# Kernel optimization log

Hardware: AMD Instinct MI355X
Metric: run time of the kernel (lower is better)

The kernel has to match this reference:

```python
import jax, jax.numpy as jnp
import numpy as np

N = 100000
E = 1600000
D_IN = 64
D_OUT = 64

def setup_inputs() -> dict:
    key = jax.random.key(0)
    k1, k2, k3 = jax.random.split(key, 3)
    x = jax.random.normal(k1, (N, D_IN), dtype=jnp.float32)
    edge_index = jax.random.randint(k2, (2, E), 0, N, dtype=jnp.int32)
    W = jax.random.normal(k3, (D_IN, D_OUT), dtype=jnp.float32) * (1.0 / np.sqrt(D_IN))
    b = jnp.zeros((D_OUT,), dtype=jnp.float32)
    return {"x": x, "edge_index": edge_index, "W": W, "b": b}

def reference(x, edge_index, W, b):
    # GCN.forward in eval mode: dropout is identity; GCNConv with
    # normalize=True, add_self_loops=True, edge_weight=None (all ones).
    loop = jnp.arange(N, dtype=edge_index.dtype)
    row = jnp.concatenate([edge_index[0], loop])   # source nodes, [E+N]
    col = jnp.concatenate([edge_index[1], loop])   # target nodes, [E+N]
    ew = jnp.ones(row.shape[0], dtype=x.dtype)
    # symmetric normalization: deg over targets, norm = d^-1/2[row] * d^-1/2[col]
    deg = jax.ops.segment_sum(ew, col, num_segments=N)
    dinv = jnp.where(deg > 0, jax.lax.rsqrt(deg), 0.0)
    norm = dinv[row] * dinv[col]                   # [E+N]
    h = x @ W                                      # [N, D_OUT] dense GEMM first (PyG order)
    msg = h[row] * norm[:, None]                   # gather + scale, [E+N, D_OUT]
    out = jax.ops.segment_sum(msg, col, num_segments=N)  # scatter-add aggregate
    return out + b
```

## Files before the change

kernel.cpp:

```cpp
#include <hip/hip_runtime.h>
#include <hip/hip_fp16.h>
#include <math.h>

constexpr int D = 64;
constexpr int BNODES = 128;
constexpr int BSHIFT = 7;
constexpr int BSTRIDE = 3072;
constexpr int PCHUNK = 4096;
constexpr int NB_MAX = 1024;

typedef _Float16 half8 __attribute__((ext_vector_type(8)));
typedef float floatx4 __attribute__((ext_vector_type(4)));

__global__ __launch_bounds__(256) void k_init(const float* __restrict__ W,
                                              __half* __restrict__ Wt,
                                              int* __restrict__ bcur, int NB) {
    const int i = blockIdx.x * 256 + threadIdx.x;
    if (i < NB) bcur[i] = i * BSTRIDE;
    if (i < D * D) {
        const int j = i >> 6;
        const int k = i & 63;
        Wt[i] = __float2half(W[k * D + j]);
    }
}

__global__ __launch_bounds__(512) void k_partition(
        const int* __restrict__ ei, int* __restrict__ bcur,
        unsigned* __restrict__ ebuf, int E, int NB) {
    __shared__ int lh[NB_MAX];
    __shared__ int lb[NB_MAX];
    __shared__ int cc[PCHUNK];
    const int t = threadIdx.x;
    for (int j = t; j < NB; j += 512) lh[j] = 0;
    __syncthreads();
    const int e0 = blockIdx.x * PCHUNK;
    const int e1 = min(e0 + PCHUNK, E);
    const bool full = (e1 - e0 == PCHUNK);

    if (full) {
        const int4* cp = reinterpret_cast<const int4*>(ei + E + e0);
        const int4 ca = cp[t];
        const int4 cb = cp[t + 512];
        reinterpret_cast<int4*>(cc)[t]       = ca;
        reinterpret_cast<int4*>(cc)[t + 512] = cb;
        atomicAdd(&lh[ca.x >> BSHIFT], 1); atomicAdd(&lh[ca.y >> BSHIFT], 1);
        atomicAdd(&lh[ca.z >> BSHIFT], 1); atomicAdd(&lh[ca.w >> BSHIFT], 1);
        atomicAdd(&lh[cb.x >> BSHIFT], 1); atomicAdd(&lh[cb.y >> BSHIFT], 1);
        atomicAdd(&lh[cb.z >> BSHIFT], 1); atomicAdd(&lh[cb.w >> BSHIFT], 1);
    } else {
        for (int e = e0 + t; e < e1; e += 512) {
            const int c = ei[E + e];
            cc[e - e0] = c;
            atomicAdd(&lh[c >> BSHIFT], 1);
        }
    }
    __syncthreads();
    for (int j = t; j < NB; j += 512) {
        const int n = lh[j];
        lb[j] = n ? atomicAdd(&bcur[j], n) : 0;
        lh[j] = 0;
    }
    __syncthreads();

    if (full) {
        const int4* rp = reinterpret_cast<const int4*>(ei + e0);
        const int4 ra = rp[t];
        const int4 rb = rp[t + 512];
        const int r8[8] = {ra.x, ra.y, ra.z, ra.w, rb.x, rb.y, rb.z, rb.w};
#pragma unroll
        for (int k = 0; k < 8; ++k) {
            const int ci = (k < 4) ? (4 * t + k) : (2048 + 4 * t + (k - 4));
            const int c = cc[ci];
            const int bkt = c >> BSHIFT;
            const int rank = atomicAdd(&lh[bkt], 1);
            const int pos = lb[bkt] + rank;
            if (pos < (bkt + 1) * BSTRIDE)
                ebuf[pos] = ((unsigned)r8[k] << BSHIFT) | (unsigned)(c & (BNODES - 1));
        }
    } else {
        for (int e = e0 + t; e < e1; e += 512) {
            const int r = ei[e];
            const int c = cc[e - e0];
            const int bkt = c >> BSHIFT;
            const int rank = atomicAdd(&lh[bkt], 1);
            const int pos = lb[bkt] + rank;
            if (pos < (bkt + 1) * BSTRIDE)
                ebuf[pos] = ((unsigned)r << BSHIFT) | (unsigned)(c & (BNODES - 1));
        }
    }
}

__global__ __launch_bounds__(512) void k_gemm_fused(
        const float* __restrict__ x, const __half* __restrict__ Wt,
        const unsigned* __restrict__ ebuf, const int* __restrict__ bcur,
        __half* __restrict__ gh, int N) {
    __shared__ int lh[BNODES];
    const int j = blockIdx.x;
    const int t = threadIdx.x;
    const int base = j << BSHIFT;
    const int s0 = j * BSTRIDE;
    const int s1 = min(bcur[j], s0 + BSTRIDE);

    if (t < BNODES) lh[t] = 0;
    __syncthreads();
    for (int i = s0 + t; i < s1; i += 512)
        atomicAdd(&lh[ebuf[i] & (BNODES - 1)], 1);
    __syncthreads();

    const int wave = t >> 6;
    const int node16 = base + wave * 16;
    if (node16 >= N) return;
    const int lane = t & 63;
    const int r16  = lane & 15;
    const int kq   = lane >> 4;

    const _Float16* wt = (const _Float16*)Wt;
    half8 bf[4][2];
#pragma unroll
    for (int jt = 0; jt < 4; ++jt)
#pragma unroll
        for (int s = 0; s < 2; ++s)
            bf[jt][s] = *(const half8*)(wt + (jt * 16 + r16) * D + s * 32 + kq * 8);

    half8 af[2];
#pragma unroll
    for (int s = 0; s < 2; ++s) {
        const float4* xp = reinterpret_cast<const float4*>(
            x + (size_t)(node16 + r16) * D + s * 32 + kq * 8);
        const float4 x0 = xp[0];
        const float4 x1 = xp[1];
        half8 a;
        a[0] = (_Float16)x0.x; a[1] = (_Float16)x0.y;
        a[2] = (_Float16)x0.z; a[3] = (_Float16)x0.w;
        a[4] = (_Float16)x1.x; a[5] = (_Float16)x1.y;
        a[6] = (_Float16)x1.z; a[7] = (_Float16)x1.w;
        af[s] = a;
    }

    floatx4 acc[4];
#pragma unroll
    for (int jt = 0; jt < 4; ++jt) {
        acc[jt] = (floatx4){0.f, 0.f, 0.f, 0.f};
        acc[jt] = __builtin_amdgcn_mfma_f32_16x16x32_f16(af[0], bf[jt][0], acc[jt], 0, 0, 0);
        acc[jt] = __builtin_amdgcn_mfma_f32_16x16x32_f16(af[1], bf[jt][1], acc[jt], 0, 0, 0);
    }

#pragma unroll
    for (int r = 0; r < 4; ++r) {
        const int nl = wave * 16 + kq * 4 + r;
        const int node = base + nl;
        const float dinv = rsqrtf((float)(lh[nl] + 1));
#pragma unroll
        for (int jt = 0; jt < 4; ++jt)
            gh[(size_t)node * D + jt * 16 + r16] = __float2half(acc[jt][r] * dinv);
    }
}

__global__ __launch_bounds__(512) void k_breduce(
        const unsigned* __restrict__ ebuf, const int* __restrict__ bcur,
        const __half* __restrict__ gh, const float* __restrict__ b,
        float* __restrict__ out, int N) {
    __shared__ int srcLDS[BSTRIDE];
    __shared__ int lh[BNODES];
    __shared__ int st[BNODES];
    __shared__ int lcur[BNODES];
    const int j = blockIdx.x;
    const int t = threadIdx.x;
    const int s0 = j * BSTRIDE;
    const int s1 = min(bcur[j], s0 + BSTRIDE);
    const int base = j << BSHIFT;
    const int nn = min(BNODES, N - base);

    if (t < BNODES) lh[t] = 0;
    __syncthreads();
    for (int i = s0 + t; i < s1; i += 512)
        atomicAdd(&lh[ebuf[i] & (BNODES - 1)], 1);
    __syncthreads();
    if (t < 64) {
        const int v0 = lh[2 * t];
        const int v1 = lh[2 * t + 1];
        int s = v0 + v1;
#pragma unroll
        for (int off = 1; off < 64; off <<= 1) {
            const int y = __shfl_up(s, off, 64);
            if (t >= off) s += y;
        }
        const int excl = s - (v0 + v1);
        st[2 * t] = excl;         st[2 * t + 1] = excl + v0;
        lcur[2 * t] = excl;       lcur[2 * t + 1] = excl + v0;
    }
    __syncthreads();
    for (int i = s0 + t; i < s1; i += 512) {
        const unsigned code = ebuf[i];
        const int c = code & (BNODES - 1);
        const int rank = atomicAdd(&lcur[c], 1);
        srcLDS[rank] = (int)(code >> BSHIFT);
    }
    __syncthreads();

    const int g8 = t >> 3;
    const int fl = t & 7;

    const uint4* g4 = reinterpret_cast<const uint4*>(gh);
    const float4* b4 = reinterpret_cast<const float4*>(b);
    float4* o4 = reinterpret_cast<float4*>(out);
    const __half2 z = __float2half2_rn(0.f);
    const float4 bb0 = b4[fl * 2];
    const float4 bb1 = b4[fl * 2 + 1];

#pragma unroll
    for (int q = 0; q < 2; ++q) {
        const int nl = q * 64 + g8;
        if (nl >= nn) continue;
        const int node = base + nl;
        const int start = st[nl];
        const int num = lh[nl];

        const uint4 su = g4[(size_t)node * 8 + fl];
        __half2 a0 = *(const __half2*)&su.x, a1 = *(const __half2*)&su.y;
        __half2 a2 = *(const __half2*)&su.z, a3 = *(const __half2*)&su.w;
        __half2 p0 = z, p1 = z, p2 = z, p3 = z;
        __half2 q0 = z, q1 = z, q2 = z, q3 = z;
        __half2 s0h = z, s1h = z, s2h = z, s3h = z;

        int i = start;
        const int end = start + num;
        for (; i + 4 <= end; i += 4) {
            const int r0 = srcLDS[i];
            const int r1 = srcLDS[i + 1];
            const int r2 = srcLDS[i + 2];
            const int r3 = srcLDS[i + 3];
            const uint4 u0 = g4[(size_t)r0 * 8 + fl];
            const uint4 u1 = g4[(size_t)r1 * 8 + fl];
            const uint4 u2 = g4[(size_t)r2 * 8 + fl];
            const uint4 u3 = g4[(size_t)r3 * 8 + fl];
            a0 = __hadd2(a0, *(const __half2*)&u0.x);
            a1 = __hadd2(a1, *(const __half2*)&u0.y);
            a2 = __hadd2(a2, *(const __half2*)&u0.z);
            a3 = __hadd2(a3, *(const __half2*)&u0.w);
            p0 = __hadd2(p0, *(const __half2*)&u1.x);
            p1 = __hadd2(p1, *(const __half2*)&u1.y);
            p2 = __hadd2(p2, *(const __half2*)&u1.z);
            p3 = __hadd2(p3, *(const __half2*)&u1.w);
            q0 = __hadd2(q0, *(const __half2*)&u2.x);
            q1 = __hadd2(q1, *(const __half2*)&u2.y);
            q2 = __hadd2(q2, *(const __half2*)&u2.z);
            q3 = __hadd2(q3, *(const __half2*)&u2.w);
            s0h = __hadd2(s0h, *(const __half2*)&u3.x);
            s1h = __hadd2(s1h, *(const __half2*)&u3.y);
            s2h = __hadd2(s2h, *(const __half2*)&u3.z);
            s3h = __hadd2(s3h, *(const __half2*)&u3.w);
        }
        for (; i < end; ++i) {
            const int r = srcLDS[i];
            const uint4 u = g4[(size_t)r * 8 + fl];
            a0 = __hadd2(a0, *(const __half2*)&u.x);
            a1 = __hadd2(a1, *(const __half2*)&u.y);
            a2 = __hadd2(a2, *(const __half2*)&u.z);
            a3 = __hadd2(a3, *(const __half2*)&u.w);
        }
        a0 = __hadd2(__hadd2(a0, p0), __hadd2(q0, s0h));
        a1 = __hadd2(__hadd2(a1, p1), __hadd2(q1, s1h));
        a2 = __hadd2(__hadd2(a2, p2), __hadd2(q2, s2h));
        a3 = __hadd2(__hadd2(a3, p3), __hadd2(q3, s3h));

        const float dinv = rsqrtf((float)(num + 1));
        const float2 f0 = __half22float2(a0);
        const float2 f1 = __half22float2(a1);
        const float2 f2 = __half22float2(a2);
        const float2 f3 = __half22float2(a3);
        float4 o0, o1;
        o0.x = fmaf(dinv, f0.x, bb0.x); o0.y = fmaf(dinv, f0.y, bb0.y);
        o0.z = fmaf(dinv, f1.x, bb0.z); o0.w = fmaf(dinv, f1.y, bb0.w);
        o1.x = fmaf(dinv, f2.x, bb1.x); o1.y = fmaf(dinv, f2.y, bb1.y);
        o1.z = fmaf(dinv, f3.x, bb1.z); o1.w = fmaf(dinv, f3.y, bb1.w);
        o4[(size_t)node * 16 + fl * 2]     = o0;
        o4[(size_t)node * 16 + fl * 2 + 1] = o1;
    }
}

extern "C" void kernel_launch(void* const* d_in, const int* in_sizes, int n_in,
                              void* d_out, int out_size, void* d_ws, size_t ws_size,
                              hipStream_t stream) {
    const float* x  = (const float*)d_in[0];
    const int*   ei = (const int*)d_in[1];
    const float* W  = (const float*)d_in[2];
    const float* b  = (const float*)d_in[3];
    float* out = (float*)d_out;

    const int N = in_sizes[0] / D;
    const int E = in_sizes[1] / 2;
    const int NB = (N + BNODES - 1) >> BSHIFT;
    const int blocksP = (E + PCHUNK - 1) / PCHUNK;

    __half*   gh   = (__half*)d_ws;
    __half*   Wt   = gh + (size_t)N * D;
    unsigned* ebuf = (unsigned*)(Wt + D * D);
    int*      bcur = (int*)(ebuf + (size_t)NB * BSTRIDE);

    k_init      <<<16, 256, 0, stream>>>(W, Wt, bcur, NB);
    k_partition <<<blocksP, 512, 0, stream>>>(ei, bcur, ebuf, E, NB);
    k_gemm_fused<<<NB, 512, 0, stream>>>(x, Wt, ebuf, bcur, gh, N);
    k_breduce   <<<NB, 512, 0, stream>>>(ebuf, bcur, gh, b, out, N);
}
```

Measured before the change: 78.95 us.

## Drop init kernel, fold W transpose into partition, unroll gather loop by eight

Removes the separate init kernel: bucket cursors are zeroed with a memset and become relative offsets, and the W transpose to fp16 runs in block 0 of the partition kernel. In the reduce kernel, the self-loop seed row is loaded before the LDS scatter so its latency overlaps, and the neighbor gather loop gains an 8-wide unrolled stage for more loads in flight. This trades a launch for a memset plus more register pressure in the reduce kernel.

```diff
diff --git a/kernel.cpp b/kernel.cpp
--- a/kernel.cpp
+++ b/kernel.cpp
@@ -12,25 +12,20 @@
 typedef _Float16 half8 __attribute__((ext_vector_type(8)));
 typedef float floatx4 __attribute__((ext_vector_type(4)));
 
-__global__ __launch_bounds__(256) void k_init(const float* __restrict__ W,
-                                              __half* __restrict__ Wt,
-                                              int* __restrict__ bcur, int NB) {
-    const int i = blockIdx.x * 256 + threadIdx.x;
-    if (i < NB) bcur[i] = i * BSTRIDE;
-    if (i < D * D) {
-        const int j = i >> 6;
-        const int k = i & 63;
-        Wt[i] = __float2half(W[k * D + j]);
-    }
-}
-
 __global__ __launch_bounds__(512) void k_partition(
-        const int* __restrict__ ei, int* __restrict__ bcur,
+        const int* __restrict__ ei, const float* __restrict__ W,
+        __half* __restrict__ Wt, int* __restrict__ bcur,
         unsigned* __restrict__ ebuf, int E, int NB) {
     __shared__ int lh[NB_MAX];
     __shared__ int lb[NB_MAX];
     __shared__ int cc[PCHUNK];
     const int t = threadIdx.x;
+
+    if (blockIdx.x == 0) {
+        for (int i = t; i < D * D; i += 512)
+            Wt[i] = __float2half(W[(i & 63) * D + (i >> 6)]);
+    }
+
     for (int j = t; j < NB; j += 512) lh[j] = 0;
     __syncthreads();
     const int e0 = blockIdx.x * PCHUNK;
@@ -57,7 +52,7 @@
     __syncthreads();
     for (int j = t; j < NB; j += 512) {
         const int n = lh[j];
-        lb[j] = n ? atomicAdd(&bcur[j], n) : 0;
+        lb[j] = n ? (j * BSTRIDE + atomicAdd(&bcur[j], n)) : 0;
         lh[j] = 0;
     }
     __syncthreads();
@@ -99,7 +94,7 @@
     const int t = threadIdx.x;
     const int base = j << BSHIFT;
     const int s0 = j * BSTRIDE;
-    const int s1 = min(bcur[j], s0 + BSTRIDE);
+    const int s1 = s0 + min(bcur[j], BSTRIDE);
 
     if (t < BNODES) lh[t] = 0;
     __syncthreads();
@@ -167,7 +162,7 @@
     const int j = blockIdx.x;
     const int t = threadIdx.x;
     const int s0 = j * BSTRIDE;
-    const int s1 = min(bcur[j], s0 + BSTRIDE);
+    const int s1 = s0 + min(bcur[j], BSTRIDE);
     const int base = j << BSHIFT;
     const int nn = min(BNODES, N - base);
 
@@ -190,6 +185,16 @@
         lcur[2 * t] = excl;       lcur[2 * t + 1] = excl + v0;
     }
     __syncthreads();
+
+    const int g8 = t >> 3;
+    const int fl = t & 7;
+    const uint4* g4 = reinterpret_cast<const uint4*>(gh);
+
+    const int nl0 = g8, nl1 = 64 + g8;
+    uint4 seed[2];
+    seed[0] = g4[(size_t)(base + nl0) * 8 + fl];
+    if (nl1 < nn) seed[1] = g4[(size_t)(base + nl1) * 8 + fl];
+
     for (int i = s0 + t; i < s1; i += 512) {
         const unsigned code = ebuf[i];
         const int c = code & (BNODES - 1);
@@ -198,10 +203,6 @@
     }
     __syncthreads();
 
-    const int g8 = t >> 3;
-    const int fl = t & 7;
-
-    const uint4* g4 = reinterpret_cast<const uint4*>(gh);
     const float4* b4 = reinterpret_cast<const float4*>(b);
     float4* o4 = reinterpret_cast<float4*>(out);
     const __half2 z = __float2half2_rn(0.f);
@@ -216,7 +217,7 @@
         const int start = st[nl];
         const int num = lh[nl];
 
-        const uint4 su = g4[(size_t)node * 8 + fl];
+        const uint4 su = seed[q];
         __half2 a0 = *(const __half2*)&su.x, a1 = *(const __half2*)&su.y;
         __half2 a2 = *(const __half2*)&su.z, a3 = *(const __half2*)&su.w;
         __half2 p0 = z, p1 = z, p2 = z, p3 = z;
@@ -225,11 +226,55 @@
 
         int i = start;
         const int end = start + num;
+        for (; i + 8 <= end; i += 8) {
+            const int r0 = srcLDS[i],     r1 = srcLDS[i + 1];
+            const int r2 = srcLDS[i + 2], r3 = srcLDS[i + 3];
+            const int r4 = srcLDS[i + 4], r5 = srcLDS[i + 5];
+            const int r6 = srcLDS[i + 6], r7 = srcLDS[i + 7];
+            const uint4 u0 = g4[(size_t)r0 * 8 + fl];
+            const uint4 u1 = g4[(size_t)r1 * 8 + fl];
+            const uint4 u2 = g4[(size_t)r2 * 8 + fl];
+            const uint4 u3 = g4[(size_t)r3 * 8 + fl];
+            const uint4 u4 = g4[(size_t)r4 * 8 + fl];
+            const uint4 u5 = g4[(size_t)r5 * 8 + fl];
+            const uint4 u6 = g4[(size_t)r6 * 8 + fl];
+            const uint4 u7 = g4[(size_t)r7 * 8 + fl];
+            a0 = __hadd2(a0, *(const __half2*)&u0.x);
+            a1 = __hadd2(a1, *(const __half2*)&u0.y);
+            a2 = __hadd2(a2, *(const __half2*)&u0.z);
+            a3 = __hadd2(a3, *(const __half2*)&u0.w);
+            p0 = __hadd2(p0, *(const __half2*)&u1.x);
+            p1 = __hadd2(p1, *(const __half2*)&u1.y);
+            p2 = __hadd2(p2, *(const __half2*)&u1.z);
+            p3 = __hadd2(p3, *(const __half2*)&u1.w);
+            q0 = __hadd2(q0, *(const __half2*)&u2.x);
+            q1 = __hadd2(q1, *(const __half2*)&u2.y);
+            q2 = __hadd2(q2, *(const __half2*)&u2.z);
+            q3 = __hadd2(q3, *(const __half2*)&u2.w);
+            s0h = __hadd2(s0h, *(const __half2*)&u3.x);
+            s1h = __hadd2(s1h, *(const __half2*)&u3.y);
+            s2h = __hadd2(s2h, *(const __half2*)&u3.z);
+            s3h = __hadd2(s3h, *(const __half2*)&u3.w);
+            a0 = __hadd2(a0, *(const __half2*)&u4.x);
+            a1 = __hadd2(a1, *(const __half2*)&u4.y);
+            a2 = __hadd2(a2, *(const __half2*)&u4.z);
+            a3 = __hadd2(a3, *(const __half2*)&u4.w);
+            p0 = __hadd2(p0, *(const __half2*)&u5.x);
+            p1 = __hadd2(p1, *(const __half2*)&u5.y);
+            p2 = __hadd2(p2, *(const __half2*)&u5.z);
+            p3 = __hadd2(p3, *(const __half2*)&u5.w);
+            q0 = __hadd2(q0, *(const __half2*)&u6.x);
+            q1 = __hadd2(q1, *(const __half2*)&u6.y);
+            q2 = __hadd2(q2, *(const __half2*)&u6.z);
+            q3 = __hadd2(q3, *(const __half2*)&u6.w);
+            s0h = __hadd2(s0h, *(const __half2*)&u7.x);
+            s1h = __hadd2(s1h, *(const __half2*)&u7.y);
+            s2h = __hadd2(s2h, *(const __half2*)&u7.z);
+            s3h = __hadd2(s3h, *(const __half2*)&u7.w);
+        }
         for (; i + 4 <= end; i += 4) {
-            const int r0 = srcLDS[i];
-            const int r1 = srcLDS[i + 1];
-            const int r2 = srcLDS[i + 2];
-            const int r3 = srcLDS[i + 3];
+            const int r0 = srcLDS[i],     r1 = srcLDS[i + 1];
+            const int r2 = srcLDS[i + 2], r3 = srcLDS[i + 3];
             const uint4 u0 = g4[(size_t)r0 * 8 + fl];
             const uint4 u1 = g4[(size_t)r1 * 8 + fl];
             const uint4 u2 = g4[(size_t)r2 * 8 + fl];
@@ -298,8 +343,8 @@
     unsigned* ebuf = (unsigned*)(Wt + D * D);
     int*      bcur = (int*)(ebuf + (size_t)NB * BSTRIDE);
 
-    k_init      <<<16, 256, 0, stream>>>(W, Wt, bcur, NB);
-    k_partition <<<blocksP, 512, 0, stream>>>(ei, bcur, ebuf, E, NB);
+    hipMemsetAsync(bcur, 0, NB * sizeof(int), stream);
+    k_partition <<<blocksP, 512, 0, stream>>>(ei, W, Wt, bcur, ebuf, E, NB);
     k_gemm_fused<<<NB, 512, 0, stream>>>(x, Wt, ebuf, bcur, gh, N);
     k_breduce   <<<NB, 512, 0, stream>>>(ebuf, bcur, gh, b, out, N);
 }
```

Result: slower. 83.01 us (+5.1%).
